# Optimization experiments

Measured on AMD Instinct MI355X. Metric: run time of the kernel, lower is better.

The kernel has to match this reference:

```python
import jax, jax.numpy as jnp
import numpy as np

B, T, C = 2, 2048, 2048
N_HEAD = 16

def setup_inputs() -> dict:
    key = jax.random.key(0)
    k1, k2, k3 = jax.random.split(key, 3)
    scale = 1.0 / np.sqrt(C)
    return {
        "x": jax.random.normal(k1, (B, T, C), dtype=jnp.float32),
        "w_attn": jax.random.normal(k2, (C, 3 * C), dtype=jnp.float32) * scale,
        "b_attn": jnp.zeros((3 * C,), dtype=jnp.float32),
        "w_proj": jax.random.normal(k3, (C, C), dtype=jnp.float32) * scale,
        "b_proj": jnp.zeros((C,), dtype=jnp.float32),
    }

def reference(x, w_attn, b_attn, w_proj, b_proj):
    Bb, Tt, Cc = x.shape
    hd = Cc // N_HEAD  # head_size
    qkv = x @ w_attn + b_attn              # [B,T,3C]
    q, k, v = jnp.split(qkv, 3, axis=-1)
    # [B,T,C] -> [B,H,T,hd]
    def heads(t):
        return t.reshape(Bb, Tt, N_HEAD, hd).transpose(0, 2, 1, 3)
    q, k, v = heads(q), heads(k), heads(v)
    att = jnp.einsum("bhqd,bhkd->bhqk", q, k) * (hd ** -0.5)
    causal = jnp.tril(jnp.ones((Tt, Tt), dtype=bool))
    att = jnp.where(causal[None, None], att, -jnp.inf)
    att = jax.nn.softmax(att, axis=-1)
    out = jnp.einsum("bhqk,bhkd->bhqd", att, v)
    out = out.transpose(0, 2, 1, 3).reshape(Bb, Tt, Cc)
    return out @ w_proj + b_proj
```

## Files before the change

kernel.cpp:

```cpp
#include <hip/hip_runtime.h>
#include <cstdint>
#include <cstddef>

typedef __bf16 bf16_t;
typedef __bf16 bf16x8 __attribute__((ext_vector_type(8)));
typedef __bf16 bf16x4 __attribute__((ext_vector_type(4)));
typedef float floatx4 __attribute__((ext_vector_type(4)));

#define B_  2
#define T_  2048
#define C_  2048
#define H_  16
#define HD_ 128

#define K_ATTN_SCALE (0.08838834764831843f * 1.44269504088896f)

__device__ __forceinline__ void async_copy16(const void* g, void* l) {
  __builtin_amdgcn_global_load_lds((const __attribute__((address_space(1))) unsigned int*)g,
                                   (__attribute__((address_space(3))) unsigned int*)l,
                                   16, 0, 0);
}

__global__ __launch_bounds__(256) void cvt_f32_bf16(const float* __restrict__ in,
                                                    bf16_t* __restrict__ out, int n4) {
  int i = blockIdx.x * 256 + threadIdx.x;
  if (i >= n4) return;
  const float4 v = ((const float4*)in)[i];
  bf16x4 o;
  o[0] = (bf16_t)v.x; o[1] = (bf16_t)v.y; o[2] = (bf16_t)v.z; o[3] = (bf16_t)v.w;
  ((bf16x4*)out)[i] = o;
}

__global__ __launch_bounds__(256) void transpose_cvt(const float* __restrict__ W,
                                                     bf16_t* __restrict__ Wt,
                                                     int Kd, int Nd) {
  __shared__ float tile[32][33];
  const int tx = threadIdx.x, ty = threadIdx.y;
  const int n0 = blockIdx.x * 32, k0 = blockIdx.y * 32;
#pragma unroll
  for (int j = ty; j < 32; j += 8)
    tile[j][tx] = W[(size_t)(k0 + j) * Nd + n0 + tx];
  __syncthreads();
#pragma unroll
  for (int j = ty; j < 32; j += 8)
    Wt[(size_t)(n0 + j) * Kd + k0 + tx] = (bf16_t)tile[tx][j];
}

#define GBM 256
#define GBN 256
#define GBK 32

__global__ __launch_bounds__(512, 2) void gemm_qkv(
    const bf16_t* __restrict__ A, const bf16_t* __restrict__ Bt,
    const float* __restrict__ bias,
    bf16_t* __restrict__ Qo, bf16_t* __restrict__ Ko, bf16_t* __restrict__ Vo,
    int K) {
  __shared__ __align__(16) char smem[131072];
  const int tid = threadIdx.x;
  const int wave = tid >> 6, lane = tid & 63;
  const int quad = lane >> 4, l15 = lane & 15;
  const int wm = wave >> 2, wn = wave & 3;
  const int bm = blockIdx.y * GBM, bn = blockIdx.x * GBN;

  const bf16_t* asrc[2];
  const bf16_t* bsrc[2];
#pragma unroll
  for (int l = 0; l < 2; ++l) {
    int p = l * 8192 + tid * 16;
    int r = p >> 6;
    int c = ((p >> 4) & 3) ^ (r & 3);
    asrc[l] = A  + (size_t)(bm + r) * K + c * 8;
    bsrc[l] = Bt + (size_t)(bn + r) * K + c * 8;
  }

  auto stageA = [&](int buf, int k0) {
    char* As = smem + buf * 32768;
#pragma unroll
    for (int l = 0; l < 2; ++l)
      async_copy16(asrc[l] + k0, As + l * 8192 + tid * 16);
  };
  auto stageB = [&](int buf, int k0) {
    char* Bs = smem + buf * 32768 + 16384;
#pragma unroll
    for (int l = 0; l < 2; ++l)
      async_copy16(bsrc[l] + k0, Bs + l * 8192 + tid * 16);
  };

  const int sx = (l15 & 3) << 4;
  const int cq = quad * 16;
  const int arow = (wm * 128 + l15) * 64;
  const int brow = (wn * 64 + l15) * 64;

  floatx4 acc[8][4] = {};
  bf16x8 af[8], bfr[4];

  stageA(0, 0); stageB(0, 0);
  stageA(1, GBK); stageB(1, GBK);
  asm volatile("s_waitcnt vmcnt(4)" ::: "memory");
  __builtin_amdgcn_s_barrier();

  const int NT = K / GBK;
  int cur = 0;
  for (int t = 0; t < NT; ++t) {
    const char* As = smem + cur * 32768;
    const char* Bs = As + 16384;
    int nxt = cur + 2; if (nxt >= 3) nxt -= 3;
    const bool st = (t + 2 < NT);

#pragma unroll
    for (int j = 0; j < 4; ++j)
      bfr[j] = *(const bf16x8*)(Bs + brow + j * 16 * 64 + (cq ^ sx));
#pragma unroll
    for (int i = 0; i < 4; ++i)
      af[i] = *(const bf16x8*)(As + arow + i * 16 * 64 + (cq ^ sx));
    if (st) stageA(nxt, (t + 2) * GBK);
    __builtin_amdgcn_sched_barrier(0);
    __builtin_amdgcn_s_barrier();
    asm volatile("s_waitcnt lgkmcnt(0)" ::: "memory");
    __builtin_amdgcn_sched_barrier(0);
    __builtin_amdgcn_s_setprio(1);
#pragma unroll
    for (int i = 0; i < 4; ++i)
#pragma unroll
      for (int j = 0; j < 4; ++j)
        acc[i][j] = __builtin_amdgcn_mfma_f32_16x16x32_bf16(af[i], bfr[j], acc[i][j], 0, 0, 0);
    __builtin_amdgcn_s_setprio(0);
    __builtin_amdgcn_sched_barrier(0);
    __builtin_amdgcn_s_barrier();

#pragma unroll
    for (int i = 4; i < 8; ++i)
      af[i] = *(const bf16x8*)(As + arow + i * 16 * 64 + (cq ^ sx));
    if (st) stageB(nxt, (t + 2) * GBK);
    __builtin_amdgcn_sched_barrier(0);
    __builtin_amdgcn_s_barrier();
    asm volatile("s_waitcnt lgkmcnt(0)" ::: "memory");
    __builtin_amdgcn_sched_barrier(0);
    __builtin_amdgcn_s_setprio(1);
#pragma unroll
    for (int i = 4; i < 8; ++i)
#pragma unroll
      for (int j = 0; j < 4; ++j)
        acc[i][j] = __builtin_amdgcn_mfma_f32_16x16x32_bf16(af[i], bfr[j], acc[i][j], 0, 0, 0);
    __builtin_amdgcn_s_setprio(0);
    __builtin_amdgcn_sched_barrier(0);

    if (t < NT - 2) {
      asm volatile("s_waitcnt vmcnt(4)" ::: "memory");
    } else if (t == NT - 2) {
      asm volatile("s_waitcnt vmcnt(0)" ::: "memory");
    }
    __builtin_amdgcn_s_barrier();
    cur = cur + 1; if (cur >= 3) cur -= 3;
  }

  float bias_r[4];
#pragma unroll
  for (int j = 0; j < 4; ++j)
    bias_r[j] = bias[bn + wn * 64 + j * 16 + l15];

  if (bn < 2 * C_) {
    const int which = bn >> 11;
    bf16_t* dst0 = which ? Ko : Qo;
    const float scl = which ? 1.0f : K_ATTN_SCALE;
#pragma unroll
    for (int i = 0; i < 8; ++i) {
      const int m = bm + wm * 128 + i * 16 + quad * 4;
      const int b = m >> 11, tq = m & 2047;
#pragma unroll
      for (int j = 0; j < 4; ++j) {
        const int n = bn + wn * 64 + j * 16 + l15;
        const int cc = n & 2047;
        const int h = cc >> 7, d = cc & 127;
        bf16_t* dst = dst0 + (((size_t)(b * H_ + h)) * T_ + tq) * HD_ + d;
#pragma unroll
        for (int r = 0; r < 4; ++r)
          dst[(size_t)r * HD_] = (bf16_t)((acc[i][j][r] + bias_r[j]) * scl);
      }
    }
  } else {
    __syncthreads();
    bf16_t* vt = (bf16_t*)smem;
#pragma unroll
    for (int i = 0; i < 8; ++i) {
      const int tl = wm * 128 + i * 16 + quad * 4;
#pragma unroll
      for (int j = 0; j < 4; ++j) {
        const int dl = wn * 64 + j * 16 + l15;
        const int sw = 8 * (dl & 15);
#pragma unroll
        for (int r = 0; r < 4; ++r)
          vt[dl * 256 + ((tl + r) ^ sw)] = (bf16_t)(acc[i][j][r] + bias_r[j]);
      }
    }
    __syncthreads();
    const int dr = tid >> 1, half = tid & 1;
    const int h = ((bn - 2 * C_) >> 7) + (dr >> 7);
    const int b = bm >> 11, t0g = bm & 2047;
    bf16_t* dst = Vo + ((size_t)(b * H_ + h) * HD_ + (dr & 127)) * T_ + t0g;
#pragma unroll
    for (int cc2 = 0; cc2 < 16; ++cc2) {
      const int c = half * 16 + cc2;
      uint4 v = *(const uint4*)&vt[dr * 256 + ((c ^ (dr & 15)) * 8)];
      *(uint4*)(dst + c * 8) = v;
    }
  }
}

#define TM 128
#define TN 128
#define BK 64

__global__ __launch_bounds__(256) void gemm_proj(
    const bf16_t* __restrict__ A, const bf16_t* __restrict__ Bt,
    const float* __restrict__ bias, float* __restrict__ Cout,
    int M, int N, int K) {
  __shared__ __align__(16) char smem[32768];
  bf16_t (*As)[BK] = (bf16_t(*)[BK])smem;
  bf16_t (*Bs)[BK] = (bf16_t(*)[BK])(smem + 16384);
  const int tid = threadIdx.x;
  const int wave = tid >> 6, lane = tid & 63;
  const int quad = lane >> 4, l15 = lane & 15;
  const int bm = blockIdx.y * TM, bn = blockIdx.x * TN;
  const int wm = (wave >> 1) * 64, wn = (wave & 1) * 64;
  const int sw = l15 & 7;

  floatx4 acc[4][4] = {};

  for (int k0 = 0; k0 < K; k0 += BK) {
#pragma unroll
    for (int it = 0; it < 4; ++it) {
      int p = it * 4096 + tid * 16;
      int r = p >> 7;
      int cg = ((p >> 4) & 7) ^ (r & 7);
      async_copy16(A + (size_t)(bm + r) * K + k0 + cg * 8, (char*)&As[0][0] + p);
      async_copy16(Bt + (size_t)(bn + r) * K + k0 + cg * 8, (char*)&Bs[0][0] + p);
    }
    __syncthreads();
#pragma unroll
    for (int kc = 0; kc < 2; ++kc) {
      const int cidx = (kc * 4 + quad) ^ sw;
      bf16x8 af[4], bf[4];
#pragma unroll
      for (int i = 0; i < 4; ++i)
        af[i] = *(const bf16x8*)&As[wm + i * 16 + l15][cidx * 8];
#pragma unroll
      for (int j = 0; j < 4; ++j)
        bf[j] = *(const bf16x8*)&Bs[wn + j * 16 + l15][cidx * 8];
#pragma unroll
      for (int i = 0; i < 4; ++i)
#pragma unroll
        for (int j = 0; j < 4; ++j)
          acc[i][j] = __builtin_amdgcn_mfma_f32_16x16x32_bf16(af[i], bf[j], acc[i][j], 0, 0, 0);
    }
    __syncthreads();
  }

#pragma unroll
  for (int i = 0; i < 4; ++i) {
#pragma unroll
    for (int j = 0; j < 4; ++j) {
#pragma unroll
      for (int r = 0; r < 4; ++r) {
        int m = bm + wm + i * 16 + quad * 4 + r;
        int n = bn + wn + j * 16 + l15;
        Cout[(size_t)m * N + n] = acc[i][j][r] + bias[n];
      }
    }
  }
}

__global__ __launch_bounds__(256) void attn(const bf16_t* __restrict__ Q,
                                            const bf16_t* __restrict__ Kg,
                                            const bf16_t* __restrict__ Vt,
                                            bf16_t* __restrict__ O) {
  __shared__ bf16_t Ks[2][64][128];
  __shared__ bf16_t Vs[2][128][64];
  const int tid = threadIdx.x;
  const int wave = tid >> 6, lane = tid & 63;
  const int quad = lane >> 4, l15 = lane & 15;
  const int j = blockIdx.x;
  const int bh = blockIdx.y;
  const int b = bh >> 4, h = bh & 15;
  const int qtA = 31 - j, qtB = j;
  const int nchA = qtA + 1, nchB = qtB + 1;
  const int q0A = qtA * 64 + wave * 16;
  const int q0B = qtB * 64 + wave * 16;

  const bf16_t* Qh = Q + (size_t)bh * T_ * HD_;
  const bf16_t* Kh = Kg + (size_t)bh * T_ * HD_;
  const bf16_t* Vh = Vt + (size_t)bh * HD_ * T_;

  bf16x8 qfA[4], qfB[4];
#pragma unroll
  for (int kk = 0; kk < 4; ++kk) {
    qfA[kk] = *(const bf16x8*)(Qh + (size_t)(q0A + l15) * HD_ + kk * 32 + quad * 8);
    qfB[kk] = *(const bf16x8*)(Qh + (size_t)(q0B + l15) * HD_ + kk * 32 + quad * 8);
  }

  floatx4 oaccA[8] = {}, oaccB[8] = {};
  float l_A = 0.0f, l_B = 0.0f;

  union PU { bf16x4 v; long long u; };
  union PF { long long u[2]; bf16x8 v; };
  const int lo = ((lane & 16) << 1) + l15;

  auto stage = [&](int buf, int kt0) {
#pragma unroll
    for (int it = 0; it < 4; ++it) {
      int p = it * 4096 + tid * 16;
      int r = p >> 8;
      int cg = ((p >> 4) & 15) ^ (r & 15);
      async_copy16(Kh + (size_t)(kt0 + r) * HD_ + cg * 8, (char*)&Ks[buf][0][0] + p);
    }
#pragma unroll
    for (int it = 0; it < 4; ++it) {
      int p = it * 4096 + tid * 16;
      int r = p >> 7;
      int cg = ((p >> 4) & 7) ^ (r & 7);
      async_copy16(Vh + (size_t)r * T_ + kt0 + cg * 8, (char*)&Vs[buf][0][0] + p);
    }
  };

  auto step = [&](int buf, const bf16x8* qf, floatx4* oacc, float& l_i, int q0, int kt0,
                  bool mask) {
    floatx4 s[4] = {{}, {}, {}, {}};
#pragma unroll
    for (int st = 0; st < 4; ++st) {
#pragma unroll
      for (int kk = 0; kk < 4; ++kk) {
        bf16x8 kf = *(const bf16x8*)&Ks[buf][st * 16 + l15][(((kk * 4 + quad) ^ l15) & 15) * 8];
        s[st] = __builtin_amdgcn_mfma_f32_16x16x32_bf16(kf, qf[kk], s[st], 0, 0, 0);
      }
    }
    float ps = 0.0f;
    long long pu[4];
#pragma unroll
    for (int st = 0; st < 4; ++st) {
      PU t;
#pragma unroll
      for (int r = 0; r < 4; ++r) {
        float val = s[st][r];
        if (mask) {
          int kt = kt0 + st * 16 + quad * 4 + r;
          val = (kt <= q0 + l15) ? val : -3.0e38f;
        }
        float p = exp2f(val);
        ps += p;
        t.v[r] = (bf16_t)p;
      }
      pu[st] = t.u;
    }
    ps += __shfl_xor(ps, 16);
    ps += __shfl_xor(ps, 32);
    l_i += ps;
#pragma unroll
    for (int bb = 0; bb < 2; ++bb) {
      long long lo0 = __shfl(pu[2 * bb], lo);
      long long hi0 = __shfl(pu[2 * bb], lo + 16);
      long long lo1 = __shfl(pu[2 * bb + 1], lo);
      long long hi1 = __shfl(pu[2 * bb + 1], lo + 16);
      PF pf;
      pf.u[0] = (quad >= 2) ? lo1 : lo0;
      pf.u[1] = (quad >= 2) ? hi1 : hi0;
#pragma unroll
      for (int dt = 0; dt < 8; ++dt) {
        bf16x8 vf = *(const bf16x8*)&Vs[buf][dt * 16 + l15][(((bb * 4 + quad) ^ l15) & 7) * 8];
        oacc[dt] = __builtin_amdgcn_mfma_f32_16x16x32_bf16(pf.v, vf, oacc[dt], 0, 0, 0);
      }
    }
  };

  stage(0, 0);
  for (int ch = 0; ch < nchA; ++ch) {
    __syncthreads();
    if (ch + 1 < nchA) stage((ch + 1) & 1, (ch + 1) * 64);
    const int kt0 = ch * 64;
    const int buf = ch & 1;
    step(buf, qfA, oaccA, l_A, q0A, kt0, ch == nchA - 1);
    if (ch < nchB) step(buf, qfB, oaccB, l_B, q0B, kt0, ch == nchB - 1);
  }

  float lrA[4], lrB[4];
#pragma unroll
  for (int r = 0; r < 4; ++r) {
    lrA[r] = __shfl(l_A, quad * 4 + r);
    lrB[r] = __shfl(l_B, quad * 4 + r);
  }
#pragma unroll
  for (int dt = 0; dt < 8; ++dt) {
#pragma unroll
    for (int r = 0; r < 4; ++r) {
      int d = dt * 16 + l15;
      int qa = q0A + quad * 4 + r;
      int qb = q0B + quad * 4 + r;
      O[((size_t)(b * T_ + qa)) * C_ + h * HD_ + d] = (bf16_t)(oaccA[dt][r] / lrA[r]);
      O[((size_t)(b * T_ + qb)) * C_ + h * HD_ + d] = (bf16_t)(oaccB[dt][r] / lrB[r]);
    }
  }
}

extern "C" void kernel_launch(void* const* d_in, const int* in_sizes, int n_in,
                              void* d_out, int out_size, void* d_ws, size_t ws_size,
                              hipStream_t stream) {
  const float* x      = (const float*)d_in[0];
  const float* w_attn = (const float*)d_in[1];
  const float* b_attn = (const float*)d_in[2];
  const float* w_proj = (const float*)d_in[3];
  const float* b_proj = (const float*)d_in[4];
  float* out = (float*)d_out;

  char* p = (char*)d_ws;
  bf16_t* xb  = (bf16_t*)p; p += (size_t)4096 * 2048 * 2;
  bf16_t* waT = (bf16_t*)p; p += (size_t)6144 * 2048 * 2;
  bf16_t* wpT = (bf16_t*)p; p += (size_t)2048 * 2048 * 2;
  bf16_t* Qb  = (bf16_t*)p; p += (size_t)32 * 2048 * 128 * 2;
  bf16_t* Kb  = (bf16_t*)p; p += (size_t)32 * 2048 * 128 * 2;
  bf16_t* Vb  = (bf16_t*)p; p += (size_t)32 * 2048 * 128 * 2;
  bf16_t* Ob  = (bf16_t*)p; p += (size_t)4096 * 2048 * 2;

  cvt_f32_bf16<<<8192, 256, 0, stream>>>(x, xb, 2097152);
  transpose_cvt<<<dim3(6144 / 32, 2048 / 32), dim3(32, 8), 0, stream>>>(w_attn, waT, 2048, 6144);
  transpose_cvt<<<dim3(2048 / 32, 2048 / 32), dim3(32, 8), 0, stream>>>(w_proj, wpT, 2048, 2048);

  gemm_qkv<<<dim3(6144 / GBN, 4096 / GBM), 512, 0, stream>>>(
      xb, waT, b_attn, Qb, Kb, Vb, 2048);

  attn<<<dim3(16, 32), 256, 0, stream>>>(Qb, Kb, Vb, Ob);

  gemm_proj<<<dim3(2048 / TN, 4096 / TM), 256, 0, stream>>>(
      Ob, wpT, b_proj, out, 4096, 2048, 2048);
}
```

Baseline: 434.4 us.

## Restructure QKV GEMM pipeline to double-buffered 64-wide K tiles

Replaces the triple-buffered 32-wide K pipeline in the QKV projection GEMM with a double-buffered 64-wide K tile, split into two 32-wide sub-slices. Loads for the next tile are issued alongside compute, and the fragment register count is halved by reusing af[4]. The LDS swizzle changes to XOR with (row>>1)&3, which is meant to cut bank conflicts. Fewer outer iterations reduce loop and barrier overhead per unit of K, but each iteration has more barriers and a longer prefetch distance, and the LDS footprint of 128KB stays the same.

Result: faster. 423.3 us (-2.5%).

```diff
diff --git a/kernel.cpp b/kernel.cpp
--- a/kernel.cpp
+++ b/kernel.cpp
@@ -20,6 +20,10 @@
                                    (__attribute__((address_space(3))) unsigned int*)l,
                                    16, 0, 0);
 }
+
+#define BAR()   asm volatile("s_barrier" ::: "memory")
+#define LGKM0() do { asm volatile("s_waitcnt lgkmcnt(0)" ::: "memory"); \
+                     __builtin_amdgcn_sched_barrier(0); } while (0)
 
 __global__ __launch_bounds__(256) void cvt_f32_bf16(const float* __restrict__ in,
                                                     bf16_t* __restrict__ out, int n4) {
@@ -48,7 +52,7 @@
 
 #define GBM 256
 #define GBN 256
-#define GBK 32
+#define GBK 64
 
 __global__ __launch_bounds__(512, 2) void gemm_qkv(
     const bf16_t* __restrict__ A, const bf16_t* __restrict__ Bt,
@@ -68,56 +72,52 @@
   for (int l = 0; l < 2; ++l) {
     int p = l * 8192 + tid * 16;
     int r = p >> 6;
-    int c = ((p >> 4) & 3) ^ (r & 3);
+    int c = ((p >> 4) & 3) ^ ((r >> 1) & 3);
     asrc[l] = A  + (size_t)(bm + r) * K + c * 8;
     bsrc[l] = Bt + (size_t)(bn + r) * K + c * 8;
   }
 
-  auto stageA = [&](int buf, int k0) {
-    char* As = smem + buf * 32768;
+  auto stage = [&](int buf, int ks, int kofs) {
+    char* Asl = smem + buf * 65536 + ks * 16384;
+    char* Bsl = Asl + 32768;
 #pragma unroll
     for (int l = 0; l < 2; ++l)
-      async_copy16(asrc[l] + k0, As + l * 8192 + tid * 16);
+      async_copy16(asrc[l] + kofs, Asl + l * 8192 + tid * 16);
+#pragma unroll
+    for (int l = 0; l < 2; ++l)
+      async_copy16(bsrc[l] + kofs, Bsl + l * 8192 + tid * 16);
   };
-  auto stageB = [&](int buf, int k0) {
-    char* Bs = smem + buf * 32768 + 16384;
-#pragma unroll
-    for (int l = 0; l < 2; ++l)
-      async_copy16(bsrc[l] + k0, Bs + l * 8192 + tid * 16);
-  };
-
-  const int sx = (l15 & 3) << 4;
-  const int cq = quad * 16;
+
+  const int sxr = ((l15 >> 1) & 3) << 4;
+  const int cb  = (quad * 16) ^ sxr;
   const int arow = (wm * 128 + l15) * 64;
   const int brow = (wn * 64 + l15) * 64;
 
   floatx4 acc[8][4] = {};
-  bf16x8 af[8], bfr[4];
-
-  stageA(0, 0); stageB(0, 0);
-  stageA(1, GBK); stageB(1, GBK);
+  bf16x8 af[4], bfr[4];
+
+  stage(0, 0, 0);
+  stage(0, 1, 32);
   asm volatile("s_waitcnt vmcnt(4)" ::: "memory");
-  __builtin_amdgcn_s_barrier();
+  BAR();
 
   const int NT = K / GBK;
-  int cur = 0;
   for (int t = 0; t < NT; ++t) {
-    const char* As = smem + cur * 32768;
-    const char* Bs = As + 16384;
-    int nxt = cur + 2; if (nxt >= 3) nxt -= 3;
-    const bool st = (t + 2 < NT);
+    const int buf = t & 1;
+    const char* Ab = smem + buf * 65536;
+    const char* Bb = Ab + 32768;
+    const bool st = (t + 1 < NT);
+    const int nk = (t + 1) * GBK;
 
 #pragma unroll
     for (int j = 0; j < 4; ++j)
-      bfr[j] = *(const bf16x8*)(Bs + brow + j * 16 * 64 + (cq ^ sx));
-#pragma unroll
-    for (int i = 0; i < 4; ++i)
-      af[i] = *(const bf16x8*)(As + arow + i * 16 * 64 + (cq ^ sx));
-    if (st) stageA(nxt, (t + 2) * GBK);
-    __builtin_amdgcn_sched_barrier(0);
-    __builtin_amdgcn_s_barrier();
-    asm volatile("s_waitcnt lgkmcnt(0)" ::: "memory");
-    __builtin_amdgcn_sched_barrier(0);
+      bfr[j] = *(const bf16x8*)(Bb + brow + j * 1024 + cb);
+#pragma unroll
+    for (int i = 0; i < 4; ++i)
+      af[i] = *(const bf16x8*)(Ab + arow + i * 1024 + cb);
+    if (st) stage(buf ^ 1, 0, nk);
+    BAR();
+    LGKM0();
     __builtin_amdgcn_s_setprio(1);
 #pragma unroll
     for (int i = 0; i < 4; ++i)
@@ -125,33 +125,60 @@
       for (int j = 0; j < 4; ++j)
         acc[i][j] = __builtin_amdgcn_mfma_f32_16x16x32_bf16(af[i], bfr[j], acc[i][j], 0, 0, 0);
     __builtin_amdgcn_s_setprio(0);
-    __builtin_amdgcn_sched_barrier(0);
-    __builtin_amdgcn_s_barrier();
-
-#pragma unroll
-    for (int i = 4; i < 8; ++i)
-      af[i] = *(const bf16x8*)(As + arow + i * 16 * 64 + (cq ^ sx));
-    if (st) stageB(nxt, (t + 2) * GBK);
-    __builtin_amdgcn_sched_barrier(0);
-    __builtin_amdgcn_s_barrier();
-    asm volatile("s_waitcnt lgkmcnt(0)" ::: "memory");
-    __builtin_amdgcn_sched_barrier(0);
+    BAR();
+
+#pragma unroll
+    for (int i = 0; i < 4; ++i)
+      af[i] = *(const bf16x8*)(Ab + arow + 4096 + i * 1024 + cb);
+    BAR();
+    LGKM0();
     __builtin_amdgcn_s_setprio(1);
 #pragma unroll
-    for (int i = 4; i < 8; ++i)
+    for (int i = 0; i < 4; ++i)
+#pragma unroll
+      for (int j = 0; j < 4; ++j)
+        acc[4 + i][j] = __builtin_amdgcn_mfma_f32_16x16x32_bf16(af[i], bfr[j], acc[4 + i][j], 0, 0, 0);
+    __builtin_amdgcn_s_setprio(0);
+    if (t == NT - 1) {
+      asm volatile("s_waitcnt vmcnt(0)" ::: "memory");
+    } else {
+      asm volatile("s_waitcnt vmcnt(4)" ::: "memory");
+    }
+    BAR();
+
+#pragma unroll
+    for (int j = 0; j < 4; ++j)
+      bfr[j] = *(const bf16x8*)(Bb + 16384 + brow + j * 1024 + cb);
+#pragma unroll
+    for (int i = 0; i < 4; ++i)
+      af[i] = *(const bf16x8*)(Ab + 16384 + arow + i * 1024 + cb);
+    if (st) stage(buf ^ 1, 1, nk + 32);
+    BAR();
+    LGKM0();
+    __builtin_amdgcn_s_setprio(1);
+#pragma unroll
+    for (int i = 0; i < 4; ++i)
 #pragma unroll
       for (int j = 0; j < 4; ++j)
         acc[i][j] = __builtin_amdgcn_mfma_f32_16x16x32_bf16(af[i], bfr[j], acc[i][j], 0, 0, 0);
     __builtin_amdgcn_s_setprio(0);
-    __builtin_amdgcn_sched_barrier(0);
-
-    if (t < NT - 2) {
+    BAR();
+
+#pragma unroll
+    for (int i = 0; i < 4; ++i)
+      af[i] = *(const bf16x8*)(Ab + 16384 + arow + 4096 + i * 1024 + cb);
+    BAR();
+    LGKM0();
+    __builtin_amdgcn_s_setprio(1);
+#pragma unroll
+    for (int i = 0; i < 4; ++i)
+#pragma unroll
+      for (int j = 0; j < 4; ++j)
+        acc[4 + i][j] = __builtin_amdgcn_mfma_f32_16x16x32_bf16(af[i], bfr[j], acc[4 + i][j], 0, 0, 0);
+    __builtin_amdgcn_s_setprio(0);
+    if (t < NT - 1)
       asm volatile("s_waitcnt vmcnt(4)" ::: "memory");
-    } else if (t == NT - 2) {
-      asm volatile("s_waitcnt vmcnt(0)" ::: "memory");
-    }
-    __builtin_amdgcn_s_barrier();
-    cur = cur + 1; if (cur >= 3) cur -= 3;
+    BAR();
   }
 
   float bias_r[4];
```
